# Performance work log

Measured on AMD Instinct MI355X. Metric: run time of the kernel, lower is better.

The kernel has to match this reference:

```python
import jax, jax.numpy as jnp
import numpy as np

EPS = 1e-3  # Keras BatchNormalization default epsilon


def _bn(x, gamma, beta, mean, var):
    # inference batch norm, channels-last
    inv = gamma * jax.lax.rsqrt(var + EPS)
    return x * inv + (beta - mean * inv)


def setup_inputs() -> dict:
    key = jax.random.key(0)
    ks = jax.random.split(key, 13)
    B, D, H, W, C, F = 2, 48, 48, 48, 64, 128
    return {
        "x": jax.random.normal(ks[0], (B, D, H, W, C), dtype=jnp.float32),
        "dw_kernel": jax.random.normal(ks[1], (3, 3, 3, 1, C), dtype=jnp.float32) * 0.1,
        "dw_bias": jax.random.normal(ks[2], (C,), dtype=jnp.float32) * 0.1,
        "bn1_gamma": jax.random.uniform(ks[3], (C,), dtype=jnp.float32, minval=0.5, maxval=1.5),
        "bn1_beta": jax.random.normal(ks[4], (C,), dtype=jnp.float32) * 0.1,
        "bn1_mean": jax.random.normal(ks[5], (C,), dtype=jnp.float32) * 0.1,
        "bn1_var": jax.random.uniform(ks[6], (C,), dtype=jnp.float32, minval=0.5, maxval=1.5),
        "pw_kernel": jax.random.normal(ks[7], (C, F), dtype=jnp.float32) * 0.1,
        "pw_bias": jax.random.normal(ks[8], (F,), dtype=jnp.float32) * 0.1,
        "bn2_gamma": jax.random.uniform(ks[9], (F,), dtype=jnp.float32, minval=0.5, maxval=1.5),
        "bn2_beta": jax.random.normal(ks[10], (F,), dtype=jnp.float32) * 0.1,
        "bn2_mean": jax.random.normal(ks[11], (F,), dtype=jnp.float32) * 0.1,
        "bn2_var": jax.random.uniform(ks[12], (F,), dtype=jnp.float32, minval=0.5, maxval=1.5),
    }


def reference(x, dw_kernel, dw_bias, bn1_gamma, bn1_beta, bn1_mean, bn1_var,
              pw_kernel, pw_bias, bn2_gamma, bn2_beta, bn2_mean, bn2_var):
    C = x.shape[-1]
    # True depthwise conv3d (replaces the per-channel Python loop of Conv3D(1,...))
    y = jax.lax.conv_general_dilated(
        x, dw_kernel,
        window_strides=(1, 1, 1), padding="SAME",
        dimension_numbers=("NDHWC", "DHWIO", "NDHWC"),
        feature_group_count=C,
    ) + dw_bias
    y = jax.nn.relu(_bn(y, bn1_gamma, bn1_beta, bn1_mean, bn1_var))
    # pointwise 1x1x1 conv == channel GEMM
    z = jnp.einsum("bdhwc,cf->bdhwf", y, pw_kernel) + pw_bias
    z = jax.nn.relu(_bn(z, bn2_gamma, bn2_beta, bn2_mean, bn2_var))
    return z
```

## Files before the change

### kernel.cpp

```cpp
#include <hip/hip_runtime.h>
#include <hip/hip_bf16.h>

#define EPS 1e-3f

typedef __attribute__((ext_vector_type(8))) short short8;
typedef __attribute__((ext_vector_type(4))) float v4f;

__device__ __forceinline__ unsigned short f2bf(float f) {
    unsigned int u = __float_as_uint(f);
    unsigned int r = (u + 0x7fffu + ((u >> 16) & 1u)) >> 16;
    return (unsigned short)r;
}

__global__ __launch_bounds__(256) void prep_kernel(
    const float* __restrict__ dwb,
    const float* __restrict__ g1, const float* __restrict__ b1,
    const float* __restrict__ m1, const float* __restrict__ v1,
    const float* __restrict__ pw, const float* __restrict__ pwb,
    const float* __restrict__ g2, const float* __restrict__ b2,
    const float* __restrict__ m2, const float* __restrict__ v2,
    float* __restrict__ scale1, float* __restrict__ shift1,
    float* __restrict__ s2, float* __restrict__ t2,
    unsigned short* __restrict__ Wt)
{
    int tid = threadIdx.x;
    if (blockIdx.x == 0) {
        if (tid < 64) {
            float inv = g1[tid] * rsqrtf(v1[tid] + EPS);
            scale1[tid] = inv;
            shift1[tid] = dwb[tid] * inv + b1[tid] - m1[tid] * inv;
        }
        if (tid < 128) {
            float inv = g2[tid] * rsqrtf(v2[tid] + EPS);
            s2[tid] = inv;
            t2[tid] = pwb[tid] * inv + b2[tid] - m2[tid] * inv;
        }
    }
    int idx = blockIdx.x * 256 + tid;
    int j     = idx & 7;
    int lane  = (idx >> 3) & 63;
    int kstep = (idx >> 9) & 1;
    int ntile = idx >> 10;
    int k = kstep * 32 + (lane >> 4) * 8 + j;
    int f = ntile * 16 + (lane & 15);
    Wt[idx] = f2bf(pw[k * 128 + f]);
}

__global__ __launch_bounds__(256, 3) void fused_kernel(
    const float* __restrict__ x,
    const float* __restrict__ wgt,
    const float* __restrict__ scale1,
    const float* __restrict__ shift1,
    const unsigned short* __restrict__ Wt,
    const float* __restrict__ s2,
    const float* __restrict__ t2,
    float* __restrict__ out)
{
    __shared__ float wS[27 * 64];
    __shared__ float sS[64];
    __shared__ float tS[64];
    __shared__ float s2S[128];
    __shared__ float t2S[128];
    __shared__ unsigned short yS[2][64 * 72];

    int tid = threadIdx.x;
    for (int i = tid; i < 27 * 64; i += 256) wS[i] = wgt[i];
    if (tid < 64) { sS[tid] = scale1[tid]; tS[tid] = shift1[tid]; }
    if (tid < 128) { s2S[tid] = s2[tid]; t2S[tid] = t2[tid]; }
    __syncthreads();

    int n   = blockIdx.x;
    int g   = (n & 7) * 144 + (n >> 3);
    int bdg = g / 36;
    int hw  = g % 36;
    int b    = bdg >> 4;
    int dgrp = bdg & 15;
    int d0   = dgrp * 3;
    int w0  = (hw % 3) * 16;
    int h0  = (hw / 3) * 4;

    int tx = tid & 15;
    int ty = tid >> 4;
    int c0 = tx * 4;
    int wq = ty & 3;
    int rh = ty >> 2;

    int wv   = tid >> 6;
    int lane = tid & 63;
    int lrow = lane & 15;
    int quad = lane >> 4;

    int w0t = w0 + wq * 4;
    float mwL = (w0t >= 1)  ? 1.f : 0.f;
    float mwR = (w0t <= 43) ? 1.f : 0.f;
    int wcl[6];
    #pragma unroll
    for (int p = 0; p < 6; ++p)
        wcl[p] = min(max(w0t - 1 + p, 0), 47) * 64;

    int h = h0 + rh;
    bool hok[3];
    int  hcl[3];
    #pragma unroll
    for (int hh = 0; hh < 3; ++hh) {
        int zh = h + hh - 1;
        hok[hh] = (zh >= 0 && zh < 48);
        hcl[hh] = min(max(zh, 0), 47) * 48 * 64;
    }

    float4 acc[3][4];
    #pragma unroll
    for (int a = 0; a < 3; ++a)
        #pragma unroll
        for (int r = 0; r < 4; ++r) acc[a][r] = make_float4(0.f, 0.f, 0.f, 0.f);

    #pragma unroll
    for (int k = 0; k < 5; ++k) {
        int s = d0 - 1 + k;
        bool s_ok = (s >= 0) && (s < 48);

        if (s_ok) {
            const float* dp = x + ((long)(b * 48 + s) * 48 * 48) * 64 + c0;
            #pragma unroll
            for (int hh = 0; hh < 3; ++hh) {
                if (hok[hh]) {
                    const float* rowp = dp + hcl[hh];
                    float4 xv[6];
                    #pragma unroll
                    for (int p = 0; p < 6; ++p)
                        xv[p] = *(const float4*)(rowp + wcl[p]);
                    xv[0].x *= mwL; xv[0].y *= mwL; xv[0].z *= mwL; xv[0].w *= mwL;
                    xv[5].x *= mwR; xv[5].y *= mwR; xv[5].z *= mwR; xv[5].w *= mwR;
                    #pragma unroll
                    for (int m = 0; m < 3; ++m) {
                        if (m >= k - 2 && m <= k) {
                            const int wz = k - m;
                            #pragma unroll
                            for (int ww = 0; ww < 3; ++ww) {
                                const float4 wvv = *(const float4*)(&wS[((wz * 3 + hh) * 3 + ww) * 64 + c0]);
                                #pragma unroll
                                for (int r = 0; r < 4; ++r) {
                                    acc[m][r].x += xv[r + ww].x * wvv.x;
                                    acc[m][r].y += xv[r + ww].y * wvv.y;
                                    acc[m][r].z += xv[r + ww].z * wvv.z;
                                    acc[m][r].w += xv[r + ww].w * wvv.w;
                                }
                            }
                        }
                    }
                }
            }
        }

        if (k >= 2) {
            const int m = k - 2;
            const int bu = m & 1;

            {
                float4 s1 = *(const float4*)(&sS[c0]);
                float4 t1 = *(const float4*)(&tS[c0]);
                #pragma unroll
                for (int r = 0; r < 4; ++r) {
                    ushort4 o;
                    o.x = f2bf(fmaxf(acc[m][r].x * s1.x + t1.x, 0.f));
                    o.y = f2bf(fmaxf(acc[m][r].y * s1.y + t1.y, 0.f));
                    o.z = f2bf(fmaxf(acc[m][r].z * s1.z + t1.z, 0.f));
                    o.w = f2bf(fmaxf(acc[m][r].w * s1.w + t1.w, 0.f));
                    *(ushort4*)(&yS[bu][(ty * 4 + r) * 72 + c0]) = o;
                }
            }
            __syncthreads();

            const short8 a0 = *(const short8*)(&yS[bu][(wv * 16 + lrow) * 72 + quad * 8]);
            const short8 a1 = *(const short8*)(&yS[bu][(wv * 16 + lrow) * 72 + 32 + quad * 8]);

            v4f gacc[8];
            #pragma unroll
            for (int nn = 0; nn < 8; ++nn) gacc[nn] = (v4f){0.f, 0.f, 0.f, 0.f};

            #pragma unroll
            for (int nn = 0; nn < 8; ++nn) {
                short8 b0 = *(const short8*)(Wt + ((nn * 2 + 0) * 64 + lane) * 8);
                short8 b1 = *(const short8*)(Wt + ((nn * 2 + 1) * 64 + lane) * 8);
                gacc[nn] = __builtin_amdgcn_mfma_f32_16x16x32_bf16(a0, b0, gacc[nn], 0, 0, 0);
                gacc[nn] = __builtin_amdgcn_mfma_f32_16x16x32_bf16(a1, b1, gacc[nn], 0, 0, 0);
            }

            int d = d0 + m;
            long base_out = ((((long)b * 48 + d) * 48 + (h0 + wv)) * 48 + w0) * 128;
            #pragma unroll
            for (int nn = 0; nn < 8; ++nn) {
                int f = nn * 16 + lrow;
                float sf = s2S[f];
                float tf = t2S[f];
                #pragma unroll
                for (int r = 0; r < 4; ++r) {
                    float v = fmaxf(gacc[nn][r] * sf + tf, 0.f);
                    out[base_out + (quad * 4 + r) * 128 + f] = v;
                }
            }
        }
    }
}

extern "C" void kernel_launch(void* const* d_in, const int* in_sizes, int n_in,
                              void* d_out, int out_size, void* d_ws, size_t ws_size,
                              hipStream_t stream)
{
    const float* x   = (const float*)d_in[0];
    const float* dwk = (const float*)d_in[1];
    const float* dwb = (const float*)d_in[2];
    const float* g1  = (const float*)d_in[3];
    const float* b1  = (const float*)d_in[4];
    const float* m1  = (const float*)d_in[5];
    const float* v1  = (const float*)d_in[6];
    const float* pw  = (const float*)d_in[7];
    const float* pwb = (const float*)d_in[8];
    const float* g2  = (const float*)d_in[9];
    const float* b2  = (const float*)d_in[10];
    const float* m2  = (const float*)d_in[11];
    const float* v2  = (const float*)d_in[12];

    float* outp = (float*)d_out;

    float* scale1 = (float*)d_ws;
    float* shift1 = scale1 + 64;
    float* s2     = scale1 + 128;
    float* t2     = scale1 + 256;
    unsigned short* Wt = (unsigned short*)((char*)d_ws + 2048);

    hipLaunchKernelGGL(prep_kernel, dim3(32), dim3(256), 0, stream,
                       dwb, g1, b1, m1, v1, pw, pwb, g2, b2, m2, v2,
                       scale1, shift1, s2, t2, Wt);

    hipLaunchKernelGGL(fused_kernel, dim3(1152), dim3(256), 0, stream,
                       x, dwk, scale1, shift1, Wt, s2, t2, outp);
}
```

Measured before the change: 206.5 us.

## Software-pipeline pointwise GEMM one depth slice behind depthwise conv loads

Restructures the depth loop so the MFMA pointwise GEMM and output stores for slice m run one iteration later, before the next slice's global loads are issued. All 18 input float4 loads per slice are hoisted into one batch separated by sched_barriers, so memory latency can overlap the GEMM and store work. The __syncthreads is replaced by an explicit lgkmcnt wait plus s_barrier. This raises register pressure (18 float4 live) under launch_bounds(256,3), and relies on the double-buffered yS to stay race-free with the shifted consumer.

```diff
diff --git a/kernel.cpp b/kernel.cpp
--- a/kernel.cpp
+++ b/kernel.cpp
@@ -115,22 +115,67 @@
         for (int r = 0; r < 4; ++r) acc[a][r] = make_float4(0.f, 0.f, 0.f, 0.f);
 
     #pragma unroll
-    for (int k = 0; k < 5; ++k) {
+    for (int k = 0; k < 6; ++k) {
         int s = d0 - 1 + k;
-        bool s_ok = (s >= 0) && (s < 48);
-
+        bool s_ok = (k <= 4) && (s >= 0) && (s < 48);
+
+        if (k >= 3) {
+            const int m = k - 3;
+            const int bu = m & 1;
+
+            const short8 a0 = *(const short8*)(&yS[bu][(wv * 16 + lrow) * 72 + quad * 8]);
+            const short8 a1 = *(const short8*)(&yS[bu][(wv * 16 + lrow) * 72 + 32 + quad * 8]);
+
+            v4f gacc[8];
+            #pragma unroll
+            for (int nn = 0; nn < 8; ++nn) gacc[nn] = (v4f){0.f, 0.f, 0.f, 0.f};
+
+            #pragma unroll
+            for (int nn = 0; nn < 8; ++nn) {
+                short8 b0 = *(const short8*)(Wt + ((nn * 2 + 0) * 64 + lane) * 8);
+                short8 b1 = *(const short8*)(Wt + ((nn * 2 + 1) * 64 + lane) * 8);
+                gacc[nn] = __builtin_amdgcn_mfma_f32_16x16x32_bf16(a0, b0, gacc[nn], 0, 0, 0);
+                gacc[nn] = __builtin_amdgcn_mfma_f32_16x16x32_bf16(a1, b1, gacc[nn], 0, 0, 0);
+            }
+
+            int d = d0 + m;
+            long base_out = ((((long)b * 48 + d) * 48 + (h0 + wv)) * 48 + w0) * 128;
+            #pragma unroll
+            for (int nn = 0; nn < 8; ++nn) {
+                int f = nn * 16 + lrow;
+                float sf = s2S[f];
+                float tf = t2S[f];
+                #pragma unroll
+                for (int r = 0; r < 4; ++r) {
+                    float v = fmaxf(gacc[nn][r] * sf + tf, 0.f);
+                    out[base_out + (quad * 4 + r) * 128 + f] = v;
+                }
+            }
+        }
+        __builtin_amdgcn_sched_barrier(0);
+
+        float4 xv[18];
         if (s_ok) {
             const float* dp = x + ((long)(b * 48 + s) * 48 * 48) * 64 + c0;
             #pragma unroll
             for (int hh = 0; hh < 3; ++hh) {
+                const float* rowp = dp + hcl[hh];
+                #pragma unroll
+                for (int p = 0; p < 6; ++p)
+                    xv[hh * 6 + p] = *(const float4*)(rowp + wcl[p]);
+            }
+        }
+        __builtin_amdgcn_sched_barrier(0);
+
+        if (s_ok) {
+            #pragma unroll
+            for (int hh = 0; hh < 3; ++hh) {
                 if (hok[hh]) {
-                    const float* rowp = dp + hcl[hh];
-                    float4 xv[6];
+                    float4 xm[6];
                     #pragma unroll
-                    for (int p = 0; p < 6; ++p)
-                        xv[p] = *(const float4*)(rowp + wcl[p]);
-                    xv[0].x *= mwL; xv[0].y *= mwL; xv[0].z *= mwL; xv[0].w *= mwL;
-                    xv[5].x *= mwR; xv[5].y *= mwR; xv[5].z *= mwR; xv[5].w *= mwR;
+                    for (int p = 0; p < 6; ++p) xm[p] = xv[hh * 6 + p];
+                    xm[0].x *= mwL; xm[0].y *= mwL; xm[0].z *= mwL; xm[0].w *= mwL;
+                    xm[5].x *= mwR; xm[5].y *= mwR; xm[5].z *= mwR; xm[5].w *= mwR;
                     #pragma unroll
                     for (int m = 0; m < 3; ++m) {
                         if (m >= k - 2 && m <= k) {
@@ -140,10 +185,10 @@
                                 const float4 wvv = *(const float4*)(&wS[((wz * 3 + hh) * 3 + ww) * 64 + c0]);
                                 #pragma unroll
                                 for (int r = 0; r < 4; ++r) {
-                                    acc[m][r].x += xv[r + ww].x * wvv.x;
-                                    acc[m][r].y += xv[r + ww].y * wvv.y;
-                                    acc[m][r].z += xv[r + ww].z * wvv.z;
-                                    acc[m][r].w += xv[r + ww].w * wvv.w;
+                                    acc[m][r].x += xm[r + ww].x * wvv.x;
+                                    acc[m][r].y += xm[r + ww].y * wvv.y;
+                                    acc[m][r].z += xm[r + ww].z * wvv.z;
+                                    acc[m][r].w += xm[r + ww].w * wvv.w;
                                 }
                             }
                         }
@@ -152,53 +197,23 @@
             }
         }
 
-        if (k >= 2) {
+        if (k >= 2 && k <= 4) {
             const int m = k - 2;
             const int bu = m & 1;
-
-            {
-                float4 s1 = *(const float4*)(&sS[c0]);
-                float4 t1 = *(const float4*)(&tS[c0]);
-                #pragma unroll
-                for (int r = 0; r < 4; ++r) {
-                    ushort4 o;
-                    o.x = f2bf(fmaxf(acc[m][r].x * s1.x + t1.x, 0.f));
-                    o.y = f2bf(fmaxf(acc[m][r].y * s1.y + t1.y, 0.f));
-                    o.z = f2bf(fmaxf(acc[m][r].z * s1.z + t1.z, 0.f));
-                    o.w = f2bf(fmaxf(acc[m][r].w * s1.w + t1.w, 0.f));
-                    *(ushort4*)(&yS[bu][(ty * 4 + r) * 72 + c0]) = o;
-                }
-            }
-            __syncthreads();
-
-            const short8 a0 = *(const short8*)(&yS[bu][(wv * 16 + lrow) * 72 + quad * 8]);
-            const short8 a1 = *(const short8*)(&yS[bu][(wv * 16 + lrow) * 72 + 32 + quad * 8]);
-
-            v4f gacc[8];
-            #pragma unroll
-            for (int nn = 0; nn < 8; ++nn) gacc[nn] = (v4f){0.f, 0.f, 0.f, 0.f};
-
-            #pragma unroll
-            for (int nn = 0; nn < 8; ++nn) {
-                short8 b0 = *(const short8*)(Wt + ((nn * 2 + 0) * 64 + lane) * 8);
-                short8 b1 = *(const short8*)(Wt + ((nn * 2 + 1) * 64 + lane) * 8);
-                gacc[nn] = __builtin_amdgcn_mfma_f32_16x16x32_bf16(a0, b0, gacc[nn], 0, 0, 0);
-                gacc[nn] = __builtin_amdgcn_mfma_f32_16x16x32_bf16(a1, b1, gacc[nn], 0, 0, 0);
-            }
-
-            int d = d0 + m;
-            long base_out = ((((long)b * 48 + d) * 48 + (h0 + wv)) * 48 + w0) * 128;
-            #pragma unroll
-            for (int nn = 0; nn < 8; ++nn) {
-                int f = nn * 16 + lrow;
-                float sf = s2S[f];
-                float tf = t2S[f];
-                #pragma unroll
-                for (int r = 0; r < 4; ++r) {
-                    float v = fmaxf(gacc[nn][r] * sf + tf, 0.f);
-                    out[base_out + (quad * 4 + r) * 128 + f] = v;
-                }
-            }
+            float4 s1 = *(const float4*)(&sS[c0]);
+            float4 t1 = *(const float4*)(&tS[c0]);
+            #pragma unroll
+            for (int r = 0; r < 4; ++r) {
+                ushort4 o;
+                o.x = f2bf(fmaxf(acc[m][r].x * s1.x + t1.x, 0.f));
+                o.y = f2bf(fmaxf(acc[m][r].y * s1.y + t1.y, 0.f));
+                o.z = f2bf(fmaxf(acc[m][r].z * s1.z + t1.z, 0.f));
+                o.w = f2bf(fmaxf(acc[m][r].w * s1.w + t1.w, 0.f));
+                *(ushort4*)(&yS[bu][(ty * 4 + r) * 72 + c0]) = o;
+            }
+            asm volatile("s_waitcnt lgkmcnt(0)" ::: "memory");
+            __builtin_amdgcn_s_barrier();
+            __builtin_amdgcn_sched_barrier(0);
         }
     }
 }
```

After: 229.2 us. 1.11x slower.
